# Performance work log

Hardware: AMD Instinct MI355X
Metric: run time of the kernel (lower is better)

Reference implementation:

```python
import jax, jax.numpy as jnp
import numpy as np

B, S, D, K = 8, 2048, 512, 64

def setup_inputs() -> dict:
    key = jax.random.key(0)
    k1, k2, k3 = jax.random.split(key, 3)
    # glorot_uniform for weights, zeros for biases (matching Keras build)
    lim = float(np.sqrt(6.0 / (D + K)))
    return {
        "inputs": jax.random.normal(k1, (B, S, D), dtype=jnp.float32),
        "key_extract": jax.random.uniform(k2, (D, K), dtype=jnp.float32, minval=-lim, maxval=lim),
        "key_bias": jnp.zeros((1, K), dtype=jnp.float32),
        "query_extract": jax.random.uniform(k3, (D, K), dtype=jnp.float32, minval=-lim, maxval=lim),
        "query_bias": jnp.zeros((1, K), dtype=jnp.float32),
    }

def reference(inputs, key_extract, key_bias, query_extract, query_bias):
    # keys/query: [B, S, K]
    keys = jnp.einsum("bsd,dk->bsk", inputs, key_extract) + key_bias
    query = jnp.einsum("bsd,dk->bsk", inputs, query_extract) + query_bias
    # logits: [B, S, S] = query @ keys^T (no 1/sqrt(K) scaling in original)
    logits = jnp.einsum("bqk,bsk->bqs", query, keys)
    # NON-STANDARD: softmax over axis=1 (the query axis), not the last axis
    attn = jax.nn.softmax(logits, axis=1)
    # weighted_input: [B, S, D], raw inputs used as V
    return jnp.einsum("bqs,bsd->bqd", attn, inputs)
```

## Files before the change

kernel.cpp:

```cpp
#include <hip/hip_runtime.h>
#include <hip/hip_bf16.h>

#define Bn 8
#define Sn 2048
#define Dn 512
#define Kn 64

typedef _Float16 half8 __attribute__((ext_vector_type(8)));
typedef _Float16 half4v __attribute__((ext_vector_type(4)));
typedef __fp16 fp16x2 __attribute__((ext_vector_type(2)));
typedef float f32x4 __attribute__((ext_vector_type(4)));

#define MFMA16(a,b,c) __builtin_amdgcn_mfma_f32_16x16x32_f16(a,b,c,0,0,0)
#define LOG2E 1.4426950408889634f
#define EXP2(x) __builtin_amdgcn_exp2f(x)

__device__ __forceinline__ void glds16(const void* g, void* l){
    __builtin_amdgcn_global_load_lds(
        (const __attribute__((address_space(1))) unsigned int*)g,
        (__attribute__((address_space(3))) unsigned int*)l, 16, 0, 0);
}

__device__ __forceinline__ half8 ldfrag(const _Float16* base, int row, int k8){
    const int scol = k8 ^ (row & 7);
    return *(const half8*)((const char*)base + row*128 + scol*16);
}


__global__ __launch_bounds__(256) void wtrans_kernel(
    const float* __restrict__ Wk, const float* __restrict__ Wq,
    _Float16* __restrict__ Wt16)
{
    const int n = blockIdx.x;
    const int t = threadIdx.x;
    const float* src = (n < 64) ? Wq : Wk;
    const int nn = n & 63;
    #pragma unroll
    for (int i = 0; i < 2; ++i){
        const int k = t + 256*i;
        Wt16[(size_t)n*Dn + k] = (_Float16)src[(size_t)k*Kn + nn];
    }
}

__global__ __launch_bounds__(256, 2) void prep_kernel(
    const float* __restrict__ X, const _Float16* __restrict__ Wt16,
    const float* __restrict__ bk, const float* __restrict__ bq,
    _Float16* __restrict__ Qh2, _Float16* __restrict__ Kh2,
    _Float16* __restrict__ Vt2)
{
    __shared__ _Float16 Xt[2][32*64];
    const int bid = blockIdx.x;
    const int b = bid & 7, sb32 = bid >> 3;
    const int tid = threadIdx.x, lane = tid & 63, w = tid >> 6;
    const int l15 = lane & 15, l4 = lane >> 4;

    const int srow = tid >> 3, sg = tid & 7;
    const float* Xs = X + ((size_t)(b*Sn + sb32*32) + srow)*Dn + sg*8;
    const int sdst = srow*128 + (((sg ^ (srow & 7) ^ (srow >> 3)) & 7) * 16);

    const int n0 = w*32 + l15;
    const _Float16* Wp0 = Wt16 + (size_t)n0*Dn + l4*8;
    const _Float16* Wp1 = Wp0 + (size_t)16*Dn;

    f32x4 acc[2][2];
    #pragma unroll
    for (int i = 0; i < 2; ++i)
        #pragma unroll
        for (int j = 0; j < 2; ++j){ f32x4 z = {0.f,0.f,0.f,0.f}; acc[i][j] = z; }

    {
        const float4 v0 = *(const float4*)(Xs);
        const float4 v1 = *(const float4*)(Xs + 4);
        half8 h;
        h[0]=(_Float16)v0.x; h[1]=(_Float16)v0.y; h[2]=(_Float16)v0.z; h[3]=(_Float16)v0.w;
        h[4]=(_Float16)v1.x; h[5]=(_Float16)v1.y; h[6]=(_Float16)v1.z; h[7]=(_Float16)v1.w;
        *(half8*)((char*)Xt[0] + sdst) = h;
    }
    __syncthreads();

    const int dcol = w*16 + l15;
    #pragma unroll
    for (int kc = 0; kc < 8; ++kc){
        const _Float16* XtC = Xt[kc & 1];
        float4 nv0, nv1;
        if (kc < 7){
            nv0 = *(const float4*)(Xs + (kc+1)*64);
            nv1 = *(const float4*)(Xs + (kc+1)*64 + 4);
        }
        const half8 wf00 = *(const half8*)(Wp0 + kc*64);
        const half8 wf01 = *(const half8*)(Wp0 + kc*64 + 32);
        const half8 wf10 = *(const half8*)(Wp1 + kc*64);
        const half8 wf11 = *(const half8*)(Wp1 + kc*64 + 32);
        #pragma unroll
        for (int ks = 0; ks < 2; ++ks){
            #pragma unroll
            for (int qt = 0; qt < 2; ++qt){
                const int rw = qt*16 + l15;
                const int g = ((ks*4 + l4) ^ (rw & 7) ^ (rw >> 3)) & 7;
                const half8 a = *(const half8*)((const char*)XtC + rw*128 + g*16);
                acc[qt][0] = MFMA16(a, ks ? wf01 : wf00, acc[qt][0]);
                acc[qt][1] = MFMA16(a, ks ? wf11 : wf10, acc[qt][1]);
            }
        }
        {
            half8 hv;
            #pragma unroll
            for (int e = 0; e < 8; ++e){
                const int rw = l4*8 + e;
                const int g = ((dcol >> 3) ^ e ^ l4) & 7;
                hv[e] = XtC[rw*64 + g*8 + (dcol & 7)];
            }
            const size_t G = (((size_t)(b*32 + (sb32 >> 1))*2 + (sb32 & 1))*32 + kc*4 + w)*64 + lane;
            *(half8*)(Vt2 + G*8) = hv;
        }
        if (kc < 7){
            half8 h;
            h[0]=(_Float16)nv0.x; h[1]=(_Float16)nv0.y; h[2]=(_Float16)nv0.z; h[3]=(_Float16)nv0.w;
            h[4]=(_Float16)nv1.x; h[5]=(_Float16)nv1.y; h[6]=(_Float16)nv1.z; h[7]=(_Float16)nv1.w;
            *(half8*)((char*)Xt[(kc+1) & 1] + sdst) = h;
        }
        __syncthreads();
    }

    _Float16* tile16 = &Xt[0][0];
    #pragma unroll
    for (int qt = 0; qt < 2; ++qt){
        const int ql = qt*16 + l4*4;
        #pragma unroll
        for (int nt = 0; nt < 2; ++nt){
            const int n = w*32 + nt*16 + l15;
            const bool isQ = (n < 64);
            const float bias = isQ ? bq[n] : bk[n - 64];
            const float scale = isQ ? LOG2E : 1.0f;
            #pragma unroll
            for (int r = 0; r < 4; ++r)
                tile16[(ql + r)*128 + n] = (_Float16)((acc[qt][nt][r] + bias) * scale);
        }
    }
    __syncthreads();
    #pragma unroll
    for (int i = 0; i < 2; ++i){
        const int g = tid + 256*i;
        const int isK = g >> 8, qtl = (g >> 7) & 1, ks = (g >> 6) & 1, ln = g & 63;
        const int l4g = ln >> 4, l15g = ln & 15;
        const half8 h = *(const half8*)&tile16[(qtl*16 + l15g)*128 + isK*64 + ks*32 + l4g*8];
        const size_t tg = (size_t)b*128 + sb32*2 + qtl;
        _Float16* dst = (isK ? Kh2 : Qh2) + ((tg*2 + ks)*64 + ln)*8;
        *(half8*)dst = h;
    }
}

__global__ __launch_bounds__(512) void stats_kernel(
    const _Float16* __restrict__ Qh2, const _Float16* __restrict__ Kh2,
    float* __restrict__ Zp)
{
    __shared__ _Float16 Qs[256*64];
    const int bid = blockIdx.x;
    const int b = bid & 7, ss = (bid >> 3) & 3, qc = bid >> 5;
    const int tid = threadIdx.x, lane = tid & 63, w = tid >> 6;
    const int l15 = lane & 15, l4 = lane >> 4;

    const char* Qsrc = (const char*)Qh2 + (size_t)(b*128 + qc*16)*2048;
    #pragma unroll
    for (int i = 0; i < 4; ++i)
        glds16(Qsrc + tid*16 + i*8192, (char*)Qs + w*1024 + i*8192);

    half8 ka[4][2];
    const char* Kb = (const char*)Kh2 + (size_t)(b*128 + ss*32 + w*4)*2048 + lane*16;
    #pragma unroll
    for (int st = 0; st < 4; ++st)
        #pragma unroll
        for (int ks = 0; ks < 2; ++ks)
            ka[st][ks] = *(const half8*)(Kb + st*2048 + ks*1024);

    __syncthreads();

    const f32x4 cinit = {-64.f, -64.f, -64.f, -64.f};
    float z[4][4];
    #pragma unroll
    for (int st = 0; st < 4; ++st)
        #pragma unroll
        for (int r = 0; r < 4; ++r) z[st][r] = 0.f;

    const char* Qb = (const char*)Qs + lane*16;
    for (int qt = 0; qt < 16; ++qt){
        const half8 qb0 = *(const half8*)(Qb + qt*2048);
        const half8 qb1 = *(const half8*)(Qb + qt*2048 + 1024);
        #pragma unroll
        for (int st = 0; st < 4; ++st){
            f32x4 c = cinit;
            c = MFMA16(ka[st][0], qb0, c);
            c = MFMA16(ka[st][1], qb1, c);
            #pragma unroll
            for (int r = 0; r < 4; ++r)
                z[st][r] += EXP2(c[r]);
        }
    }
    #pragma unroll
    for (int d = 1; d < 16; d <<= 1)
        #pragma unroll
        for (int st = 0; st < 4; ++st)
            #pragma unroll
            for (int r = 0; r < 4; ++r)
                z[st][r] += __shfl_xor(z[st][r], d);
    if (l15 == 0){
        float* zp = Zp + (((size_t)(qc*8 + b)) << 11) + ss*512 + w*64 + l4*4;
        #pragma unroll
        for (int st = 0; st < 4; ++st)
            #pragma unroll
            for (int r = 0; r < 4; ++r)
                zp[st*16 + r] = z[st][r];
    }
}

__global__ __launch_bounds__(256) void csfin_kernel(
    const float* __restrict__ Zp, float* __restrict__ CS)
{
    const int idx = blockIdx.x*256 + threadIdx.x;
    float zsum = 0.f;
    #pragma unroll
    for (int qc = 0; qc < 8; ++qc)
        zsum += Zp[(qc << 14) + idx];
    CS[idx] = -(64.0f + __log2f(zsum));
}

#define WRP(PT, QT, C) do { \
    const float e0 = EXP2(C[0]); \
    const float e1 = EXP2(C[1]); \
    const float e2 = EXP2(C[2]); \
    const float e3 = EXP2(C[3]); \
    const fp16x2 plo = __builtin_amdgcn_cvt_pkrtz(e0, e1); \
    const fp16x2 phi = __builtin_amdgcn_cvt_pkrtz(e2, e3); \
    uint2 pu; \
    pu.x = __builtin_bit_cast(unsigned int, plo); \
    pu.y = __builtin_bit_cast(unsigned int, phi); \
    *(uint2*)((char*)(PT) + (QT)*2048 + pw_base) = pu; \
} while(0)

#define ABODY(KA, KAN, VB, VBN, CSA, CSN, PT) do { \
    f32x4 c0 = {CSA.x, CSA.y, CSA.z, CSA.w}; \
    f32x4 c1 = c0, c2 = c0, c3 = c0; \
    c0 = MFMA16(KA[0], qb[0][0], c0); c0 = MFMA16(KA[1], qb[0][1], c0); \
    c1 = MFMA16(KA[0], qb[1][0], c1); c1 = MFMA16(KA[1], qb[1][1], c1); \
    c2 = MFMA16(KA[0], qb[2][0], c2); c2 = MFMA16(KA[1], qb[2][1], c2); \
    c3 = MFMA16(KA[0], qb[3][0], c3); c3 = MFMA16(KA[1], qb[3][1], c3); \
    KAN[0] = *(const half8*)(Kp); \
    KAN[1] = *(const half8*)(Kp + 1024); \
    Kp += 8192; \
    CSN = *(const float4*)Cp; Cp += 64; \
    WRP(PT, 0, c0); WRP(PT, 1, c1); \
    WRP(PT, 2, c2); WRP(PT, 3, c3); \
    asm volatile("s_waitcnt lgkmcnt(0)\n\ts_barrier" ::: "memory"); \
    _Pragma("unroll") \
    for (int d_ = 0; d_ < 4; ++d_){ \
        VBN[d_]   = *(const half8*)(Vp0 + d_*1024); \
        VBN[4+d_] = *(const half8*)(Vp1 + d_*1024); \
    } \
    Vp0 += 65536; Vp1 += 65536; \
    __builtin_amdgcn_s_setprio(1); \
    { const char* PB = (const char*)(PT); \
      _Pragma("unroll") \
      for (int ks = 0; ks < 2; ++ks){ \
        const int po = ks ? paoff1 : paoff0; \
        const half8 pa0 = *(const half8*)(PB + 0*2048 + po); \
        const half8 pa1 = *(const half8*)(PB + 1*2048 + po); \
        const half8 pa2 = *(const half8*)(PB + 2*2048 + po); \
        const half8 pa3 = *(const half8*)(PB + 3*2048 + po); \
        _Pragma("unroll") \
        for (int d_ = 0; d_ < 4; ++d_){ \
            acc[0][d_] = MFMA16(pa0, VB[ks*4+d_], acc[0][d_]); \
            acc[1][d_] = MFMA16(pa1, VB[ks*4+d_], acc[1][d_]); \
            acc[2][d_] = MFMA16(pa2, VB[ks*4+d_], acc[2][d_]); \
            acc[3][d_] = MFMA16(pa3, VB[ks*4+d_], acc[3][d_]); \
        } \
      } } \
    __builtin_amdgcn_s_setprio(0); \
} while(0)

__global__ __launch_bounds__(256, 2) void attn_kernel(
    const _Float16* __restrict__ Qh2, const _Float16* __restrict__ Kh2,
    const _Float16* __restrict__ Vt2, const float* __restrict__ CS,
    float* __restrict__ out)
{
    __shared__ _Float16 Pt[2][64*64];
    const int bid = blockIdx.x;
    const int b  = bid & 7;
    const int qi = (bid >> 3) & 31;
    const int dh = bid >> 8;
    const int q0 = qi * 64;
    const int tid = threadIdx.x, lane = tid & 63, w = tid >> 6;
    const int l15 = lane & 15, l4 = lane >> 4;
    const int soff = w*16 + l4*4;
    const int sb2  = soff * 2;
    const int pw_base = l15*128 + (sb2 ^ ((l15 & 7) << 4));
    const int paoff0  = l15*128 + ((l4 ^ (l15 & 7)) << 4);
    const int paoff1  = paoff0 ^ 64;

    const size_t qgb = (size_t)b*128 + qi*4;
    half8 qb[4][2];
    #pragma unroll
    for (int qt = 0; qt < 4; ++qt)
        #pragma unroll
        for (int ks = 0; ks < 2; ++ks)
            qb[qt][ks] = *(const half8*)(Qh2 + (((qgb + qt)*2 + ks)*64 + lane)*8);

    const char* Kp  = (const char*)Kh2 + (size_t)(b*128 + w)*2048 + lane*16;
    const char* Vp0 = (const char*)Vt2 + (size_t)(b*2048 + dh*16 + w*4)*1024 + lane*16;
    const char* Vp1 = Vp0 + 32768;
    const float* Cp = CS + b*Sn + soff;

    half8 kaA[2], kaB[2], vbA[8], vbB[8];
    float4 csA, csB;
    kaA[0] = *(const half8*)(Kp);
    kaA[1] = *(const half8*)(Kp + 1024);
    Kp += 8192;
    #pragma unroll
    for (int d_ = 0; d_ < 4; ++d_){
        vbA[d_]   = *(const half8*)(Vp0 + d_*1024);
        vbA[4+d_] = *(const half8*)(Vp1 + d_*1024);
    }
    Vp0 += 65536; Vp1 += 65536;
    csA = *(const float4*)Cp; Cp += 64;

    f32x4 acc[4][4];
    #pragma unroll
    for (int i = 0; i < 4; ++i)
        #pragma unroll
        for (int j = 0; j < 4; ++j){ f32x4 zz4 = {0.f,0.f,0.f,0.f}; acc[i][j] = zz4; }

    for (int it = 0; it < 16; ++it){
        ABODY(kaA, kaB, vbA, vbB, csA, csB, Pt[0]);
        ABODY(kaB, kaA, vbB, vbA, csB, csA, Pt[1]);
    }

    float* ob = out + (size_t)(b*Sn + q0)*Dn + dh*256 + w*64;
    #pragma unroll
    for (int qt = 0; qt < 4; ++qt){
        const int q = qt*16 + l4*4;
        #pragma unroll
        for (int d_ = 0; d_ < 4; ++d_){
            #pragma unroll
            for (int r = 0; r < 4; ++r)
                ob[(size_t)(q + r)*Dn + d_*16 + l15] = acc[qt][d_][r];
        }
    }
}

extern "C" void kernel_launch(void* const* d_in, const int* in_sizes, int n_in,
                              void* d_out, int out_size, void* d_ws, size_t ws_size,
                              hipStream_t stream)
{
    const float* X  = (const float*)d_in[0];
    const float* Wk = (const float*)d_in[1];
    const float* bk = (const float*)d_in[2];
    const float* Wq = (const float*)d_in[3];
    const float* bq = (const float*)d_in[4];
    float* out = (float*)d_out;

    char* ws = (char*)d_ws;
    _Float16* Qh2  = (_Float16*)ws;
    _Float16* Kh2  = (_Float16*)(ws + ((size_t)2 << 20));
    _Float16* Vt2  = (_Float16*)(ws + ((size_t)4 << 20));
    float*    CS   = (float*)(ws + ((size_t)20 << 20));
    _Float16* Wt16 = (_Float16*)(ws + ((size_t)20 << 20) + (2 << 16));
    float*    Zp   = (float*)(ws + ((size_t)21 << 20));

    wtrans_kernel<<<dim3(128), dim3(256), 0, stream>>>(Wk, Wq, Wt16);
    prep_kernel<<<dim3(Bn*(Sn/32)), dim3(256), 0, stream>>>(X, Wt16, bk, bq, Qh2, Kh2, Vt2);
    stats_kernel<<<dim3(256), dim3(512), 0, stream>>>(Qh2, Kh2, Zp);
    csfin_kernel<<<dim3(64), dim3(256), 0, stream>>>(Zp, CS);
    attn_kernel<<<dim3(Bn*(Sn/64)*2), dim3(256), 0, stream>>>(Qh2, Kh2, Vt2, CS, out);
}
```

Measured before the change: 68.95 us.

## Split attention block across 8 waves, halving per-wave score and output work

```diff
diff --git a/kernel.cpp b/kernel.cpp
--- a/kernel.cpp
+++ b/kernel.cpp
@@ -237,26 +237,23 @@
     *(uint2*)((char*)(PT) + (QT)*2048 + pw_base) = pu; \
 } while(0)
 
-#define ABODY(KA, KAN, VB, VBN, CSA, CSN, PT) do { \
+#define ABODY(KA, KAN, CSA, CSN, PT) do { \
     f32x4 c0 = {CSA.x, CSA.y, CSA.z, CSA.w}; \
-    f32x4 c1 = c0, c2 = c0, c3 = c0; \
+    f32x4 c1 = c0; \
     c0 = MFMA16(KA[0], qb[0][0], c0); c0 = MFMA16(KA[1], qb[0][1], c0); \
     c1 = MFMA16(KA[0], qb[1][0], c1); c1 = MFMA16(KA[1], qb[1][1], c1); \
-    c2 = MFMA16(KA[0], qb[2][0], c2); c2 = MFMA16(KA[1], qb[2][1], c2); \
-    c3 = MFMA16(KA[0], qb[3][0], c3); c3 = MFMA16(KA[1], qb[3][1], c3); \
     KAN[0] = *(const half8*)(Kp); \
     KAN[1] = *(const half8*)(Kp + 1024); \
     Kp += 8192; \
     CSN = *(const float4*)Cp; Cp += 64; \
     WRP(PT, 0, c0); WRP(PT, 1, c1); \
-    WRP(PT, 2, c2); WRP(PT, 3, c3); \
     asm volatile("s_waitcnt lgkmcnt(0)\n\ts_barrier" ::: "memory"); \
-    _Pragma("unroll") \
-    for (int d_ = 0; d_ < 4; ++d_){ \
-        VBN[d_]   = *(const half8*)(Vp0 + d_*1024); \
-        VBN[4+d_] = *(const half8*)(Vp1 + d_*1024); \
-    } \
-    Vp0 += 65536; Vp1 += 65536; \
+    half8 vb[4]; \
+    vb[0] = *(const half8*)(Vp); \
+    vb[1] = *(const half8*)(Vp + 1024); \
+    vb[2] = *(const half8*)(Vp + 32768); \
+    vb[3] = *(const half8*)(Vp + 32768 + 1024); \
+    Vp += 65536; \
     __builtin_amdgcn_s_setprio(1); \
     { const char* PB = (const char*)(PT); \
       _Pragma("unroll") \
@@ -267,17 +264,17 @@
         const half8 pa2 = *(const half8*)(PB + 2*2048 + po); \
         const half8 pa3 = *(const half8*)(PB + 3*2048 + po); \
         _Pragma("unroll") \
-        for (int d_ = 0; d_ < 4; ++d_){ \
-            acc[0][d_] = MFMA16(pa0, VB[ks*4+d_], acc[0][d_]); \
-            acc[1][d_] = MFMA16(pa1, VB[ks*4+d_], acc[1][d_]); \
-            acc[2][d_] = MFMA16(pa2, VB[ks*4+d_], acc[2][d_]); \
-            acc[3][d_] = MFMA16(pa3, VB[ks*4+d_], acc[3][d_]); \
+        for (int d_ = 0; d_ < 2; ++d_){ \
+            acc[0][d_] = MFMA16(pa0, vb[ks*2+d_], acc[0][d_]); \
+            acc[1][d_] = MFMA16(pa1, vb[ks*2+d_], acc[1][d_]); \
+            acc[2][d_] = MFMA16(pa2, vb[ks*2+d_], acc[2][d_]); \
+            acc[3][d_] = MFMA16(pa3, vb[ks*2+d_], acc[3][d_]); \
         } \
       } } \
     __builtin_amdgcn_s_setprio(0); \
 } while(0)
 
-__global__ __launch_bounds__(256, 2) void attn_kernel(
+__global__ __launch_bounds__(512, 4) void attn_kernel(
     const _Float16* __restrict__ Qh2, const _Float16* __restrict__ Kh2,
     const _Float16* __restrict__ Vt2, const float* __restrict__ CS,
     float* __restrict__ out)
@@ -290,55 +287,50 @@
     const int q0 = qi * 64;
     const int tid = threadIdx.x, lane = tid & 63, w = tid >> 6;
     const int l15 = lane & 15, l4 = lane >> 4;
-    const int soff = w*16 + l4*4;
+    const int qh = w >> 2;
+    const int st = w & 3;
+    const int soff = st*16 + l4*4;
     const int sb2  = soff * 2;
-    const int pw_base = l15*128 + (sb2 ^ ((l15 & 7) << 4));
+    const int pw_base = (qh*32 + l15)*128 + (sb2 ^ ((l15 & 7) << 4));
     const int paoff0  = l15*128 + ((l4 ^ (l15 & 7)) << 4);
     const int paoff1  = paoff0 ^ 64;
 
-    const size_t qgb = (size_t)b*128 + qi*4;
-    half8 qb[4][2];
-    #pragma unroll
-    for (int qt = 0; qt < 4; ++qt)
+    const size_t qgb = (size_t)b*128 + qi*4 + qh*2;
+    half8 qb[2][2];
+    #pragma unroll
+    for (int qt = 0; qt < 2; ++qt)
         #pragma unroll
         for (int ks = 0; ks < 2; ++ks)
             qb[qt][ks] = *(const half8*)(Qh2 + (((qgb + qt)*2 + ks)*64 + lane)*8);
 
-    const char* Kp  = (const char*)Kh2 + (size_t)(b*128 + w)*2048 + lane*16;
-    const char* Vp0 = (const char*)Vt2 + (size_t)(b*2048 + dh*16 + w*4)*1024 + lane*16;
-    const char* Vp1 = Vp0 + 32768;
+    const char* Kp = (const char*)Kh2 + (size_t)(b*128 + st)*2048 + lane*16;
+    const char* Vp = (const char*)Vt2 + (size_t)(b*2048 + dh*16 + w*2)*1024 + lane*16;
     const float* Cp = CS + b*Sn + soff;
 
-    half8 kaA[2], kaB[2], vbA[8], vbB[8];
+    half8 kaA[2], kaB[2];
     float4 csA, csB;
     kaA[0] = *(const half8*)(Kp);
     kaA[1] = *(const half8*)(Kp + 1024);
     Kp += 8192;
-    #pragma unroll
-    for (int d_ = 0; d_ < 4; ++d_){
-        vbA[d_]   = *(const half8*)(Vp0 + d_*1024);
-        vbA[4+d_] = *(const half8*)(Vp1 + d_*1024);
-    }
-    Vp0 += 65536; Vp1 += 65536;
     csA = *(const float4*)Cp; Cp += 64;
 
-    f32x4 acc[4][4];
+    f32x4 acc[4][2];
     #pragma unroll
     for (int i = 0; i < 4; ++i)
         #pragma unroll
-        for (int j = 0; j < 4; ++j){ f32x4 zz4 = {0.f,0.f,0.f,0.f}; acc[i][j] = zz4; }
+        for (int j = 0; j < 2; ++j){ f32x4 zz4 = {0.f,0.f,0.f,0.f}; acc[i][j] = zz4; }
 
     for (int it = 0; it < 16; ++it){
-        ABODY(kaA, kaB, vbA, vbB, csA, csB, Pt[0]);
-        ABODY(kaB, kaA, vbB, vbA, csB, csA, Pt[1]);
-    }
-
-    float* ob = out + (size_t)(b*Sn + q0)*Dn + dh*256 + w*64;
+        ABODY(kaA, kaB, csA, csB, Pt[0]);
+        ABODY(kaB, kaA, csB, csA, Pt[1]);
+    }
+
+    float* ob = out + (size_t)(b*Sn + q0)*Dn + dh*256 + w*32;
     #pragma unroll
     for (int qt = 0; qt < 4; ++qt){
         const int q = qt*16 + l4*4;
         #pragma unroll
-        for (int d_ = 0; d_ < 4; ++d_){
+        for (int d_ = 0; d_ < 2; ++d_){
             #pragma unroll
             for (int r = 0; r < 4; ++r)
                 ob[(size_t)(q + r)*Dn + d_*16 + l15] = acc[qt][d_][r];
@@ -369,5 +361,5 @@
     prep_kernel<<<dim3(Bn*(Sn/32)), dim3(256), 0, stream>>>(X, Wt16, bk, bq, Qh2, Kh2, Vt2);
     stats_kernel<<<dim3(256), dim3(512), 0, stream>>>(Qh2, Kh2, Zp);
     csfin_kernel<<<dim3(64), dim3(256), 0, stream>>>(Zp, CS);
-    attn_kernel<<<dim3(Bn*(Sn/64)*2), dim3(256), 0, stream>>>(Qh2, Kh2, Vt2, CS, out);
-}
+    attn_kernel<<<dim3(Bn*(Sn/64)*2), dim3(512), 0, stream>>>(Qh2, Kh2, Vt2, CS, out);
+}
```

Result: slower. 73.29 us (+6.3%).

## Halve prep kernel row tile to 16 rows, doubling block count

Applied to the files above, without the earlier changes.

```diff
diff --git a/kernel.cpp b/kernel.cpp
--- a/kernel.cpp
+++ b/kernel.cpp
@@ -21,11 +21,6 @@
         (__attribute__((address_space(3))) unsigned int*)l, 16, 0, 0);
 }
 
-__device__ __forceinline__ half8 ldfrag(const _Float16* base, int row, int k8){
-    const int scol = k8 ^ (row & 7);
-    return *(const half8*)((const char*)base + row*128 + scol*16);
-}
-
 
 __global__ __launch_bounds__(256) void wtrans_kernel(
     const float* __restrict__ Wk, const float* __restrict__ Wq,
@@ -42,33 +37,36 @@
     }
 }
 
-__global__ __launch_bounds__(256, 2) void prep_kernel(
+__global__ __launch_bounds__(256) void prep_kernel(
     const float* __restrict__ X, const _Float16* __restrict__ Wt16,
     const float* __restrict__ bk, const float* __restrict__ bq,
     _Float16* __restrict__ Qh2, _Float16* __restrict__ Kh2,
     _Float16* __restrict__ Vt2)
 {
-    __shared__ _Float16 Xt[2][32*64];
+    __shared__ _Float16 Xt[2][16*64];
     const int bid = blockIdx.x;
-    const int b = bid & 7, sb32 = bid >> 3;
+    const int b = bid & 7, sb16 = bid >> 3;
     const int tid = threadIdx.x, lane = tid & 63, w = tid >> 6;
     const int l15 = lane & 15, l4 = lane >> 4;
+    const bool half1 = (tid < 128);
 
     const int srow = tid >> 3, sg = tid & 7;
-    const float* Xs = X + ((size_t)(b*Sn + sb32*32) + srow)*Dn + sg*8;
-    const int sdst = srow*128 + (((sg ^ (srow & 7) ^ (srow >> 3)) & 7) * 16);
+    const float* Xs = X + ((size_t)(b*Sn + sb16*16) + (srow & 15))*Dn + sg*8;
+    const int sdst = (srow & 15)*128 + (((sg ^ (srow & 7) ^ ((srow >> 3) & 1)) & 7) * 16);
 
     const int n0 = w*32 + l15;
     const _Float16* Wp0 = Wt16 + (size_t)n0*Dn + l4*8;
     const _Float16* Wp1 = Wp0 + (size_t)16*Dn;
 
-    f32x4 acc[2][2];
-    #pragma unroll
-    for (int i = 0; i < 2; ++i)
-        #pragma unroll
-        for (int j = 0; j < 2; ++j){ f32x4 z = {0.f,0.f,0.f,0.f}; acc[i][j] = z; }
-
-    {
+    const int dcol = tid & 63, sgrp = (tid >> 6) & 1;
+    const int soff8 = (sb16 & 3)*2 + sgrp;
+    const int vks = soff8 >> 2, vl4 = soff8 & 3;
+    const size_t Gbase = (((size_t)(b*32 + (sb16 >> 2))*2 + vks)*32)*64 + vl4*16 + (dcol & 15);
+
+    f32x4 acc[2];
+    { f32x4 z = {0.f,0.f,0.f,0.f}; acc[0] = z; acc[1] = z; }
+
+    if (half1){
         const float4 v0 = *(const float4*)(Xs);
         const float4 v1 = *(const float4*)(Xs + 4);
         half8 h;
@@ -78,12 +76,11 @@
     }
     __syncthreads();
 
-    const int dcol = w*16 + l15;
     #pragma unroll
     for (int kc = 0; kc < 8; ++kc){
         const _Float16* XtC = Xt[kc & 1];
         float4 nv0, nv1;
-        if (kc < 7){
+        if (half1 && kc < 7){
             nv0 = *(const float4*)(Xs + (kc+1)*64);
             nv1 = *(const float4*)(Xs + (kc+1)*64 + 4);
         }
@@ -93,39 +90,35 @@
         const half8 wf11 = *(const half8*)(Wp1 + kc*64 + 32);
         #pragma unroll
         for (int ks = 0; ks < 2; ++ks){
-            #pragma unroll
-            for (int qt = 0; qt < 2; ++qt){
-                const int rw = qt*16 + l15;
-                const int g = ((ks*4 + l4) ^ (rw & 7) ^ (rw >> 3)) & 7;
-                const half8 a = *(const half8*)((const char*)XtC + rw*128 + g*16);
-                acc[qt][0] = MFMA16(a, ks ? wf01 : wf00, acc[qt][0]);
-                acc[qt][1] = MFMA16(a, ks ? wf11 : wf10, acc[qt][1]);
-            }
-        }
-        {
+            const int rw = l15;
+            const int g = ((ks*4 + l4) ^ (rw & 7) ^ (rw >> 3)) & 7;
+            const half8 a = *(const half8*)((const char*)XtC + rw*128 + g*16);
+            acc[0] = MFMA16(a, ks ? wf01 : wf00, acc[0]);
+            acc[1] = MFMA16(a, ks ? wf11 : wf10, acc[1]);
+        }
+        if (half1){
             half8 hv;
             #pragma unroll
             for (int e = 0; e < 8; ++e){
-                const int rw = l4*8 + e;
-                const int g = ((dcol >> 3) ^ e ^ l4) & 7;
+                const int rw = sgrp*8 + e;
+                const int g = ((dcol >> 3) ^ e ^ sgrp) & 7;
                 hv[e] = XtC[rw*64 + g*8 + (dcol & 7)];
             }
-            const size_t G = (((size_t)(b*32 + (sb32 >> 1))*2 + (sb32 & 1))*32 + kc*4 + w)*64 + lane;
+            const size_t G = Gbase + (size_t)(kc*4 + (dcol >> 4))*64;
             *(half8*)(Vt2 + G*8) = hv;
-        }
-        if (kc < 7){
-            half8 h;
-            h[0]=(_Float16)nv0.x; h[1]=(_Float16)nv0.y; h[2]=(_Float16)nv0.z; h[3]=(_Float16)nv0.w;
-            h[4]=(_Float16)nv1.x; h[5]=(_Float16)nv1.y; h[6]=(_Float16)nv1.z; h[7]=(_Float16)nv1.w;
-            *(half8*)((char*)Xt[(kc+1) & 1] + sdst) = h;
+            if (kc < 7){
+                half8 h;
+                h[0]=(_Float16)nv0.x; h[1]=(_Float16)nv0.y; h[2]=(_Float16)nv0.z; h[3]=(_Float16)nv0.w;
+                h[4]=(_Float16)nv1.x; h[5]=(_Float16)nv1.y; h[6]=(_Float16)nv1.z; h[7]=(_Float16)nv1.w;
+                *(half8*)((char*)Xt[(kc+1) & 1] + sdst) = h;
+            }
         }
         __syncthreads();
     }
 
     _Float16* tile16 = &Xt[0][0];
-    #pragma unroll
-    for (int qt = 0; qt < 2; ++qt){
-        const int ql = qt*16 + l4*4;
+    {
+        const int ql = l4*4;
         #pragma unroll
         for (int nt = 0; nt < 2; ++nt){
             const int n = w*32 + nt*16 + l15;
@@ -134,17 +127,14 @@
             const float scale = isQ ? LOG2E : 1.0f;
             #pragma unroll
             for (int r = 0; r < 4; ++r)
-                tile16[(ql + r)*128 + n] = (_Float16)((acc[qt][nt][r] + bias) * scale);
+                tile16[(ql + r)*128 + n] = (_Float16)((acc[nt][r] + bias) * scale);
         }
     }
     __syncthreads();
-    #pragma unroll
-    for (int i = 0; i < 2; ++i){
-        const int g = tid + 256*i;
-        const int isK = g >> 8, qtl = (g >> 7) & 1, ks = (g >> 6) & 1, ln = g & 63;
-        const int l4g = ln >> 4, l15g = ln & 15;
-        const half8 h = *(const half8*)&tile16[(qtl*16 + l15g)*128 + isK*64 + ks*32 + l4g*8];
-        const size_t tg = (size_t)b*128 + sb32*2 + qtl;
+    {
+        const int isK = tid >> 7, ks = (tid >> 6) & 1, ln = tid & 63;
+        const half8 h = *(const half8*)&tile16[(ln & 15)*128 + isK*64 + ks*32 + (ln >> 4)*8];
+        const size_t tg = (size_t)b*128 + sb16;
         _Float16* dst = (isK ? Kh2 : Qh2) + ((tg*2 + ks)*64 + ln)*8;
         *(half8*)dst = h;
     }
@@ -366,7 +356,7 @@
     float*    Zp   = (float*)(ws + ((size_t)21 << 20));
 
     wtrans_kernel<<<dim3(128), dim3(256), 0, stream>>>(Wk, Wq, Wt16);
-    prep_kernel<<<dim3(Bn*(Sn/32)), dim3(256), 0, stream>>>(X, Wt16, bk, bq, Qh2, Kh2, Vt2);
+    prep_kernel<<<dim3(Bn*(Sn/16)), dim3(256), 0, stream>>>(X, Wt16, bk, bq, Qh2, Kh2, Vt2);
     stats_kernel<<<dim3(256), dim3(512), 0, stream>>>(Qh2, Kh2, Zp);
     csfin_kernel<<<dim3(64), dim3(256), 0, stream>>>(Zp, CS);
     attn_kernel<<<dim3(Bn*(Sn/64)*2), dim3(256), 0, stream>>>(Qh2, Kh2, Vt2, CS, out);
```

After: 73.73 us. 1.07x slower.
